# Optimization experiments

Measured on AMD Instinct MI355X. Metric: run time of the kernel, lower is better.

## Reference

```python
import jax, jax.numpy as jnp
import numpy as np

B, T, C = 4, 2048, 1024
H, D = 16, 64  # n_head, head_dim; H*D == C
EPS = 1e-12


def _l2norm(x):
    # matches torch F.normalize(dim=-1): x / max(||x||_2, eps)
    n = jnp.sqrt(jnp.sum(x * x, axis=-1, keepdims=True))
    return x / jnp.maximum(n, EPS)


def setup_inputs() -> dict:
    key = jax.random.key(0)
    ks = jax.random.split(key, 8)
    s = 0.02
    return {
        "x": jax.random.normal(ks[0], (B, T, C), dtype=jnp.float32),
        "Wq": jax.random.normal(ks[1], (C, C), dtype=jnp.float32) * s,
        "Wk": jax.random.normal(ks[2], (C, C), dtype=jnp.float32) * s,
        "Wv": jax.random.normal(ks[3], (C, C), dtype=jnp.float32) * s,
        "Wbeta": jax.random.normal(ks[4], (H, C), dtype=jnp.float32) * s,
        "bbeta": jnp.zeros((H,), dtype=jnp.float32),
        "Wgate": jax.random.normal(ks[5], (C, C), dtype=jnp.float32) * s,
        "Wo": jax.random.normal(ks[6], (C, C), dtype=jnp.float32) * s,
    }


def _forward(x, Wq, Wk, Wv, Wbeta, bbeta, Wgate, Wo):
    q = (x @ Wq.T).reshape(B, T, H, D)
    k = (x @ Wk.T).reshape(B, T, H, D)
    v = (x @ Wv.T).reshape(B, T, H, D)
    beta = jax.nn.sigmoid(x @ Wbeta.T + bbeta)  # (B,T,H)
    gate = jax.nn.sigmoid(x @ Wgate.T)          # (B,T,C)

    q = _l2norm(q)
    k = _l2norm(k)

    # time-major for scan: (T,B,H,D) / (T,B,H)
    qT = jnp.transpose(q, (1, 0, 2, 3))
    kT = jnp.transpose(k, (1, 0, 2, 3))
    vT = jnp.transpose(v, (1, 0, 2, 3))
    bT = jnp.transpose(beta, (1, 0, 2))

    M0 = jnp.zeros((B, H, D, D), dtype=x.dtype)

    def step(M, inp):
        q_t, k_t, v_t, b_t = inp
        o_t = jnp.einsum('bhdc,bhc->bhd', M, q_t)       # read state with q (pre-update)
        Mk = jnp.einsum('bhdc,bhc->bhd', M, k_t)
        dv = v_t - Mk                                    # delta-rule error
        M = M + b_t[..., None, None] * jnp.einsum('bhd,bhc->bhdc', dv, k_t)
        return M, o_t

    _, oT = jax.lax.scan(step, M0, (qT, kT, vT, bT))     # oT: (T,B,H,D)
    o = jnp.transpose(oT, (1, 0, 2, 3)).reshape(B, T, C)
    return (gate * o) @ Wo.T


def reference(x, Wq, Wk, Wv, Wbeta, bbeta, Wgate, Wo):
    return _forward(x, Wq, Wk, Wv, Wbeta, bbeta, Wgate, Wo)
```

## Files before the change

### kernel.cpp

```cpp
#include <hip/hip_runtime.h>
#include <cstdint>
#include <cstddef>

#define Bz 4
#define Tz 2048
#define Cz 1024
#define Hz 16
#define Dz 64
#define NTOK (Bz*Tz)
#define CHL 32
#define NCH (Tz/CHL)

typedef __attribute__((ext_vector_type(8))) short  short8;
typedef __attribute__((ext_vector_type(4))) float  floatx4;

__device__ __forceinline__ unsigned short f2bf(float x) {
  union { float f; uint32_t u; } a; a.f = x;
  uint32_t r = a.u + 0x7fffu + ((a.u >> 16) & 1u);
  return (unsigned short)(r >> 16);
}
__device__ __forceinline__ float bf2f(unsigned short u) {
  union { uint32_t i; float f; } a; a.i = ((uint32_t)u) << 16; return a.f;
}
__device__ __forceinline__ float sigmoidf_(float z) {
  return 1.0f / (1.0f + __expf(-z));
}
__device__ __forceinline__ uint32_t cvtpk_bf16(float a, float b) {
  uint32_t d;
  asm volatile("v_cvt_pk_bf16_f32 %0, %1, %2" : "=v"(d) : "v"(a), "v"(b));
  return d;
}
__device__ __forceinline__ float lo16f(uint32_t u) {
  union { uint32_t i; float f; } a; a.i = u << 16; return a.f;
}
__device__ __forceinline__ float hi16f(uint32_t u) {
  union { uint32_t i; float f; } a; a.i = u & 0xffff0000u; return a.f;
}

__device__ __forceinline__ void gload_lds16(const void* gptr, void* lptr) {
  __builtin_amdgcn_global_load_lds(
      (const __attribute__((address_space(1))) void*)(uintptr_t)gptr,
      (__attribute__((address_space(3))) void*)(uint32_t)(uintptr_t)lptr,
      16, 0, 0);
}

template<int CTRL>
__device__ __forceinline__ float dpp_addf(float x) {
  int y = __builtin_amdgcn_update_dpp(0, __float_as_int(x), CTRL, 0xF, 0xF, true);
  return x + __int_as_float(y);
}
__device__ __forceinline__ float rowsum16(float x) {
  x = dpp_addf<0xB1>(x);
  x = dpp_addf<0x4E>(x);
  x = dpp_addf<0x124>(x);
  x = dpp_addf<0x128>(x);
  return x;
}

union FragU { uint32_t u[4]; short8 s; };

__global__ __launch_bounds__(256) void cvt_bf16_kernel(const float* __restrict__ in,
                                                       unsigned short* __restrict__ out,
                                                       int n4) {
  int i = blockIdx.x * blockDim.x + threadIdx.x;
  int stride = gridDim.x * blockDim.x;
  const float4* in4 = (const float4*)in;
  ushort4* out4 = (ushort4*)out;
  for (; i < n4; i += stride) {
    float4 f = in4[i];
    ushort4 u;
    u.x = f2bf(f.x); u.y = f2bf(f.y); u.z = f2bf(f.z); u.w = f2bf(f.w);
    out4[i] = u;
  }
}

__global__ __launch_bounds__(256) void cvt_w5_kernel(
    const float* __restrict__ s0, const float* __restrict__ s1,
    const float* __restrict__ s2, const float* __restrict__ s3,
    const float* __restrict__ s4,
    unsigned short* __restrict__ d0, unsigned short* __restrict__ d1,
    unsigned short* __restrict__ d2, unsigned short* __restrict__ d3,
    unsigned short* __restrict__ d4, int n4)
{
  const int w = blockIdx.y;
  const float* s = (w == 0) ? s0 : (w == 1) ? s1 : (w == 2) ? s2 : (w == 3) ? s3 : s4;
  unsigned short* d = (w == 0) ? d0 : (w == 1) ? d1 : (w == 2) ? d2 : (w == 3) ? d3 : d4;
  int i = blockIdx.x * blockDim.x + threadIdx.x;
  if (i < n4) {
    float4 f = ((const float4*)s)[i];
    ushort4 u;
    u.x = f2bf(f.x); u.y = f2bf(f.y); u.z = f2bf(f.z); u.w = f2bf(f.w);
    ((ushort4*)d)[i] = u;
  }
}

#define VM8()  asm volatile("s_waitcnt vmcnt(8)" ::: "memory")
#define VM4()  asm volatile("s_waitcnt vmcnt(4)" ::: "memory")
#define VM0()  asm volatile("s_waitcnt vmcnt(0)" ::: "memory")
#define LGKM0() asm volatile("s_waitcnt lgkmcnt(0)" ::: "memory")
#define BARR() __builtin_amdgcn_s_barrier()

__global__ __launch_bounds__(512, 2) void gemm256_kernel(
    const unsigned short* __restrict__ A,
    const unsigned short* __restrict__ W0, const unsigned short* __restrict__ W1,
    const unsigned short* __restrict__ W2, const unsigned short* __restrict__ W3,
    void* __restrict__ O0, void* __restrict__ O1,
    void* __restrict__ O2, void* __restrict__ O3,
    int M, int N, int K, int nz_sigmoid, int norm_mask, int out_bf16)
{
  __shared__ unsigned short smem[8 * 8192];

  const int gx = gridDim.x, gz = gridDim.z;
  const int nwg = gx * gridDim.y * gz;
  int flat = (blockIdx.z * gridDim.y + blockIdx.y) * gx + blockIdx.x;
  if ((nwg & 7) == 0) flat = (flat & 7) * (nwg >> 3) + (flat >> 3);
  const int xz = gx * gz;
  const int by = flat / xz;
  const int rem = flat - by * xz;
  const int bz = rem / gx;
  const int bx = rem - bz * gx;

  const unsigned short* Bw = (bz == 0) ? W0 : (bz == 1) ? W1 : (bz == 2) ? W2 : W3;
  void* Cw = (bz == 0) ? O0 : (bz == 1) ? O1 : (bz == 2) ? O2 : O3;
  const bool act = (bz == nz_sigmoid);
  const bool donorm = (norm_mask >> bz) & 1;

  const int m0 = by * 256, n0 = bx * 256;
  const int tid = threadIdx.x;
  const int wid = tid >> 6, lane = tid & 63;
  const int wm = wid >> 2, wn = wid & 3;
  const int ml = lane & 15, kq = lane >> 4;

  const unsigned short* Ap = A  + (size_t)m0 * K;
  const unsigned short* Bp = Bw + (size_t)n0 * K;

  const int srow = wid * 16 + (lane >> 2);
  const int ss8  = ((lane & 3) ^ ((lane >> 3) & 3)) * 8;
  const int rs8  = (kq ^ ((ml >> 1) & 3)) * 8;
  const int arow = wm * 128 + ml;
  const int brow = wn * 64 + ml;

  const int NT = K >> 6;
  const int hmax = NT << 2;

  floatx4 acc[8][4];
#pragma unroll
  for (int i = 0; i < 8; ++i)
#pragma unroll
    for (int j = 0; j < 4; ++j) acc[i][j] = floatx4{0.f, 0.f, 0.f, 0.f};

#define STAGE1(hsi) do {                                                      \
    const int ht_ = (hsi) >> 2, hh_ = (hsi) & 3;                              \
    const unsigned short* p_ = (hh_ & 1) ? Bp : Ap;                           \
    const int kb_ = ht_ * 64 + (hh_ >> 1) * 32;                               \
    unsigned short* lb_ = &smem[(((ht_ & 1) << 2) + hh_) * 8192 + wid * 512]; \
    gload_lds16(p_ + (size_t)srow * K + kb_ + ss8, lb_);                      \
    gload_lds16(p_ + (size_t)(128 + srow) * K + kb_ + ss8, lb_ + 4096);       \
  } while (0)

  int hs = 0;
  for (; hs < 6 && hs < hmax; ++hs) STAGE1(hs);
  VM8();
  BARR();

#define LOAD_A(Hb, mh)                                                        \
  _Pragma("unroll") for (int i = 0; i < 4; ++i)                               \
    af[i] = *(const short8*)&Hb[(arow + (mh) * 64 + i * 16) * 32 + rs8];
#define LOAD_B(Hb)                                                            \
  _Pragma("unroll") for (int j = 0; j < 4; ++j)                               \
    bf[j] = *(const short8*)&Hb[(brow + j * 16) * 32 + rs8];
#define MFMA_Q(mh)                                                            \
  __builtin_amdgcn_s_setprio(1);                                              \
  _Pragma("unroll") for (int i = 0; i < 4; ++i)                               \
    _Pragma("unroll") for (int j = 0; j < 4; ++j)                             \
      acc[(mh) * 4 + i][j] = __builtin_amdgcn_mfma_f32_16x16x32_bf16(         \
          af[i], bf[j], acc[(mh) * 4 + i][j], 0, 0, 0);                       \
  __builtin_amdgcn_s_setprio(0);
#define STAGE_NEXT() do { if (hs < hmax) { STAGE1(hs); ++hs; } } while (0)

  short8 af[4], bf[4];
  for (int t = 0; t < NT; ++t) {
    const unsigned short* Ah0 = &smem[(((t & 1) << 2) + 0) * 8192];
    const unsigned short* Bh0 = &smem[(((t & 1) << 2) + 1) * 8192];
    const unsigned short* Ah1 = &smem[(((t & 1) << 2) + 2) * 8192];
    const unsigned short* Bh1 = &smem[(((t & 1) << 2) + 3) * 8192];

    LOAD_A(Ah0, 0); LOAD_B(Bh0);
    STAGE_NEXT();
    BARR(); LGKM0();
    MFMA_Q(0);
    BARR();

    LOAD_A(Ah0, 1);
    STAGE_NEXT();
    BARR(); LGKM0();
    MFMA_Q(1);
    if (t == NT - 1) { VM0(); } else { VM8(); }
    BARR();

    LOAD_A(Ah1, 0); LOAD_B(Bh1);
    STAGE_NEXT();
    BARR(); LGKM0();
    MFMA_Q(0);
    BARR();

    LOAD_A(Ah1, 1);
    STAGE_NEXT();
    BARR(); LGKM0();
    MFMA_Q(1);
    if (t < NT - 2) { VM8(); } else if (t == NT - 2) { VM4(); }
    BARR();
  }

  float scale[8][4];
  if (donorm) {
#pragma unroll
    for (int i = 0; i < 8; ++i) {
#pragma unroll
      for (int r = 0; r < 4; ++r) {
        float ss = 0.f;
#pragma unroll
        for (int j = 0; j < 4; ++j) ss = fmaf(acc[i][j][r], acc[i][j][r], ss);
        ss = rowsum16(ss);
        scale[i][r] = 1.0f / fmaxf(sqrtf(ss), 1e-12f);
      }
    }
  }

  const int row_base = m0 + wm * 128;
  const int col_base = n0 + wn * 64;
#pragma unroll
  for (int i = 0; i < 8; ++i) {
#pragma unroll
    for (int j = 0; j < 4; ++j) {
      const int col = col_base + j * 16 + ml;
#pragma unroll
      for (int r = 0; r < 4; ++r) {
        const int row = row_base + i * 16 + kq * 4 + r;
        float val = acc[i][j][r];
        if (donorm) val *= scale[i][r];
        if (act) val = sigmoidf_(val);
        if (out_bf16) ((unsigned short*)Cw)[(size_t)row * N + col] = f2bf(val);
        else          ((float*)Cw)[(size_t)row * N + col] = val;
      }
    }
  }
}

__global__ __launch_bounds__(256) void beta_kernel(
    const float* __restrict__ x, const float* __restrict__ Wb,
    const float* __restrict__ bb, float* __restrict__ beta_out)
{
  const int n = blockIdx.x;
  const int wid = threadIdx.x >> 6;
  const int lane = threadIdx.x & 63;
  const float* xr = x + (size_t)n * Cz;
  for (int h = wid; h < Hz; h += 4) {
    const float* wr = Wb + (size_t)h * Cz;
    float s = 0.f;
#pragma unroll 4
    for (int i = lane; i < Cz; i += 64) s = fmaf(xr[i], wr[i], s);
#pragma unroll
    for (int ofs = 32; ofs >= 1; ofs >>= 1) s += __shfl_xor(s, ofs);
    if (lane == 0) beta_out[(size_t)n * Hz + h] = sigmoidf_(s + bb[h]);
  }
}


__global__ __launch_bounds__(256) void deltachunk_phase1(
    const unsigned short* __restrict__ qb, const unsigned short* __restrict__ kb,
    const unsigned short* __restrict__ vb, const float* __restrict__ betaf,
    float* __restrict__ of,
    unsigned short* __restrict__ qtb, unsigned short* __restrict__ wbuf,
    unsigned short* __restrict__ ubuf, unsigned short* __restrict__ ktb)
{
  __shared__ unsigned short Kb[32][72], Qb[32][72], Vb[32][72];
  __shared__ float As[32][33];
  __shared__ unsigned short Sb[32][40];
  __shared__ unsigned short Us[32][72], Ws[32][72], Qts[32][72];
  __shared__ float bsh[32];

  const int bid = blockIdx.x;
  const int chain = bid & 63;
  const int chunk = bid >> 6;
  const int b = chain >> 4, h = chain & 15;
  const int tid = threadIdx.x;
  const int wid = tid >> 6, lane = tid & 63;
  const int ml = lane & 15, kq = lane >> 4;

  const size_t tok0 = (size_t)b * Tz + (size_t)chunk * CHL;
  const size_t cb = ((size_t)chain * NCH + chunk) * 2048;

  {
    const int row = tid >> 3, c8 = (tid & 7) * 8;
    const size_t ga = (tok0 + row) * Cz + h * Dz + c8;
    *(uint4*)&Qb[row][c8] = *(const uint4*)&qb[ga];
    *(uint4*)&Kb[row][c8] = *(const uint4*)&kb[ga];
    *(uint4*)&Vb[row][c8] = *(const uint4*)&vb[ga];
  }
  if (tid < 32) bsh[tid] = betaf[(tok0 + tid) * Hz + h];
  __syncthreads();

  {
    const int tr = wid & 1, tc = wid >> 1;
    floatx4 accA = {0.f,0.f,0.f,0.f}, accS = {0.f,0.f,0.f,0.f};
#pragma unroll
    for (int eh = 0; eh < 2; ++eh) {
      short8 ka = *(const short8*)&Kb[tr * 16 + ml][eh * 32 + kq * 8];
      short8 kbf = *(const short8*)&Kb[tc * 16 + ml][eh * 32 + kq * 8];
      short8 qa = *(const short8*)&Qb[tr * 16 + ml][eh * 32 + kq * 8];
      accA = __builtin_amdgcn_mfma_f32_16x16x32_bf16(ka, kbf, accA, 0, 0, 0);
      accS = __builtin_amdgcn_mfma_f32_16x16x32_bf16(qa, kbf, accS, 0, 0, 0);
    }
#pragma unroll
    for (int r = 0; r < 4; ++r) {
      int t = tr * 16 + kq * 4 + r;
      int s = tc * 16 + ml;
      As[t][s] = bsh[t] * accA[r];
      Sb[t][s] = (t > s) ? f2bf(accS[r]) : (unsigned short)0;
    }
  }
  __syncthreads();

  if (tid < 128) {
    const int j = tid;
    float x[32];
    if (j < 64) {
#pragma unroll
      for (int t = 0; t < 32; ++t) x[t] = bsh[t] * bf2f(Vb[t][j]);
    } else {
#pragma unroll
      for (int t = 0; t < 32; ++t) x[t] = bsh[t] * bf2f(Kb[t][j - 64]);
    }
#pragma unroll
    for (int t = 0; t < 31; ++t) {
      float xt = x[t];
#pragma unroll
      for (int s = t + 1; s < 32; ++s) x[s] = fmaf(-As[s][t], xt, x[s]);
    }
    if (j < 64) {
#pragma unroll
      for (int t = 0; t < 32; ++t) Us[t][j] = f2bf(x[t]);
    } else {
#pragma unroll
      for (int t = 0; t < 32; ++t) Ws[t][j - 64] = f2bf(x[t]);
    }
  }
  __syncthreads();

  {
    const int dw = wid * 16 + ml;
    FragU bu, bw;
#pragma unroll
    for (int r = 0; r < 4; ++r) {
      bu.u[r] = (uint32_t)Us[kq * 8 + 2 * r][dw] | ((uint32_t)Us[kq * 8 + 2 * r + 1][dw] << 16);
      bw.u[r] = (uint32_t)Ws[kq * 8 + 2 * r][dw] | ((uint32_t)Ws[kq * 8 + 2 * r + 1][dw] << 16);
    }
    floatx4 accO[2], accQ[2];
#pragma unroll
    for (int tt = 0; tt < 2; ++tt) { accO[tt] = floatx4{0.f,0.f,0.f,0.f}; accQ[tt] = floatx4{0.f,0.f,0.f,0.f}; }
#pragma unroll
    for (int tt = 0; tt < 2; ++tt) {
      short8 sa = *(const short8*)&Sb[tt * 16 + ml][kq * 8];
      accO[tt] = __builtin_amdgcn_mfma_f32_16x16x32_bf16(sa, bu.s, accO[tt], 0, 0, 0);
      accQ[tt] = __builtin_amdgcn_mfma_f32_16x16x32_bf16(sa, bw.s, accQ[tt], 0, 0, 0);
    }
#pragma unroll
    for (int tt = 0; tt < 2; ++tt) {
#pragma unroll
      for (int r = 0; r < 4; ++r) {
        int t = tt * 16 + kq * 4 + r;
        of[(tok0 + t) * Cz + h * Dz + dw] = accO[tt][r];
        Qts[t][dw] = f2bf(bf2f(Qb[t][dw]) - accQ[tt][r]);
      }
    }
  }

  unsigned short ktmp[8], utmp[8];
  {
    const int e = tid >> 2, tq = (tid & 3) * 8;
#pragma unroll
    for (int i2 = 0; i2 < 8; ++i2) { ktmp[i2] = Kb[tq + i2][e]; utmp[i2] = Us[tq + i2][e]; }
  }
  __syncthreads();

  {
    const int row = tid >> 3, c8 = (tid & 7) * 8;
    const size_t o16 = cb + (size_t)row * 64 + c8;
    *(uint4*)&qtb[o16]  = *(const uint4*)&Qts[row][c8];
    *(uint4*)&wbuf[o16] = *(const uint4*)&Ws[row][c8];
    const int e = tid >> 2, tq = (tid & 3) * 8;
    *(uint4*)&ktb[cb + (size_t)e * 32 + tq]  = *(const uint4*)ktmp;
    *(uint4*)&ubuf[cb + (size_t)e * 32 + tq] = *(const uint4*)utmp;
  }
}

__global__ __launch_bounds__(256) void deltachunk_phase2(
    const unsigned short* __restrict__ qtb, const unsigned short* __restrict__ wbuf,
    const unsigned short* __restrict__ ubuf, const unsigned short* __restrict__ ktb,
    float* __restrict__ o2)
{
  __shared__ unsigned short Gb[2][64][72];
  __shared__ unsigned short Ub[2][32][40];
  __shared__ unsigned short Kts[2][64][40];
  __shared__ unsigned short Mh[2][32][72], Ml[2][32][72];

  const int chain = blockIdx.x >> 1;
  const int dh = blockIdx.x & 1;
  const int b = chain >> 4, h = chain & 15;
  const int d0 = dh * 32;
  const int tid = threadIdx.x;
  const int wid = tid >> 6, lane = tid & 63;
  const int ml = lane & 15, kq = lane >> 4;
  const int iq = wid >> 1, jq = wid & 1;

  const size_t cbase = (size_t)chain * NCH * 2048;

  const int grow = tid >> 2;
  const int gc16 = (tid & 3) * 16;
  const int ke   = tid >> 2;
  const int kc8  = (tid & 3) * 8;
  const int ue   = tid >> 3;
  const int uc4  = (tid & 7) * 4;

  const unsigned short* gsrc = (grow < 32) ? qtb : wbuf;
  const size_t gsoff = (size_t)(grow & 31) * 64 + gc16;

  {
    *(uint4*)&Gb[0][grow][gc16]     = *(const uint4*)&gsrc[cbase + gsoff];
    *(uint4*)&Gb[0][grow][gc16 + 8] = *(const uint4*)&gsrc[cbase + gsoff + 8];
    *(uint4*)&Kts[0][ke][kc8]       = *(const uint4*)&ktb[cbase + (size_t)ke * 32 + kc8];
    *(uint2*)&Ub[0][ue][uc4]        = *(const uint2*)&ubuf[cbase + (size_t)(d0 + ue) * 32 + uc4];
  }
  for (int i = tid; i < 32 * 72; i += 256) { (&Mh[0][0][0])[i] = 0; (&Ml[0][0][0])[i] = 0; }
  __syncthreads();

  const int idxA = (ml + 16 * ((kq & 1) * 2)) * 4;
  const int idxB = (ml + 16 * ((kq & 1) * 2 + 1)) * 4;
  const bool hiKq = (kq >= 2);

  floatx4 mAcc[4];
#pragma unroll
  for (int a = 0; a < 4; ++a) mAcc[a] = floatx4{0.f, 0.f, 0.f, 0.f};

  for (int c = 0; c < NCH; ++c) {
    const int cbuf = c & 1, nbuf = cbuf ^ 1;
    const int mr = c & 1, mw = mr ^ 1;
    const size_t tok0 = (size_t)b * Tz + (size_t)c * CHL;

    const int cn = (c + 1 < NCH) ? c + 1 : c;
    const size_t cbn = cbase + (size_t)cn * 2048;
    uint4 sg0 = *(const uint4*)&gsrc[cbn + gsoff];
    uint4 sg1 = *(const uint4*)&gsrc[cbn + gsoff + 8];
    uint4 sk  = *(const uint4*)&ktb[cbn + (size_t)ke * 32 + kc8];
    uint2 su  = *(const uint2*)&ubuf[cbn + (size_t)(d0 + ue) * 32 + uc4];

    floatx4 g1[2];
    g1[0] = floatx4{0.f,0.f,0.f,0.f}; g1[1] = floatx4{0.f,0.f,0.f,0.f};
#pragma unroll
    for (int eh = 0; eh < 2; ++eh) {
      short8 afr0 = *(const short8*)&Gb[cbuf][iq * 32 + 0  + ml][eh * 32 + kq * 8];
      short8 afr1 = *(const short8*)&Gb[cbuf][iq * 32 + 16 + ml][eh * 32 + kq * 8];
      short8 bh = *(const short8*)&Mh[mr][jq * 16 + ml][eh * 32 + kq * 8];
      short8 bl = *(const short8*)&Ml[mr][jq * 16 + ml][eh * 32 + kq * 8];
      g1[0] = __builtin_amdgcn_mfma_f32_16x16x32_bf16(afr0, bh, g1[0], 0, 0, 0);
      g1[0] = __builtin_amdgcn_mfma_f32_16x16x32_bf16(afr0, bl, g1[0], 0, 0, 0);
      g1[1] = __builtin_amdgcn_mfma_f32_16x16x32_bf16(afr1, bh, g1[1], 0, 0, 0);
      g1[1] = __builtin_amdgcn_mfma_f32_16x16x32_bf16(afr1, bl, g1[1], 0, 0, 0);
    }

    if (iq == 0) {
#pragma unroll
      for (int ti = 0; ti < 2; ++ti)
#pragma unroll
        for (int r = 0; r < 4; ++r)
          o2[(tok0 + ti * 16 + kq * 4 + r) * Cz + h * Dz + d0 + jq * 16 + ml] = g1[ti][r];
    } else {
      uint32_t pkh[2][2], pkl[2][2];
#pragma unroll
      for (int ti = 0; ti < 2; ++ti) {
        ushort4 uu = *(const ushort4*)&Ub[cbuf][jq * 16 + ml][ti * 16 + kq * 4];
        float z0 = bf2f(uu.x) - g1[ti][0];
        float z1 = bf2f(uu.y) - g1[ti][1];
        float z2 = bf2f(uu.z) - g1[ti][2];
        float z3 = bf2f(uu.w) - g1[ti][3];
        uint32_t h01 = cvtpk_bf16(z0, z1), h23 = cvtpk_bf16(z2, z3);
        pkh[ti][0] = h01; pkh[ti][1] = h23;
        pkl[ti][0] = cvtpk_bf16(z0 - lo16f(h01), z1 - hi16f(h01));
        pkl[ti][1] = cvtpk_bf16(z2 - lo16f(h23), z3 - hi16f(h23));
      }
      FragU zh, zl;
#pragma unroll
      for (int s = 0; s < 4; ++s) {
        const int idx = (s < 2) ? idxA : idxB;
        const int rp = s & 1;
        int v0 = __builtin_amdgcn_ds_bpermute(idx, (int)pkh[0][rp]);
        int v1 = __builtin_amdgcn_ds_bpermute(idx, (int)pkh[1][rp]);
        zh.u[s] = hiKq ? (uint32_t)v1 : (uint32_t)v0;
        int w0 = __builtin_amdgcn_ds_bpermute(idx, (int)pkl[0][rp]);
        int w1 = __builtin_amdgcn_ds_bpermute(idx, (int)pkl[1][rp]);
        zl.u[s] = hiKq ? (uint32_t)w1 : (uint32_t)w0;
      }
#pragma unroll
      for (int et = 0; et < 4; ++et) {
        short8 kfr = *(const short8*)&Kts[cbuf][et * 16 + ml][kq * 8];
        mAcc[et] = __builtin_amdgcn_mfma_f32_16x16x32_bf16(kfr, zh.s, mAcc[et], 0, 0, 0);
        mAcc[et] = __builtin_amdgcn_mfma_f32_16x16x32_bf16(kfr, zl.s, mAcc[et], 0, 0, 0);
      }
#pragma unroll
      for (int et = 0; et < 4; ++et) {
        float m0 = mAcc[et][0], m1 = mAcc[et][1], m2 = mAcc[et][2], m3 = mAcc[et][3];
        uint32_t h01 = cvtpk_bf16(m0, m1), h23 = cvtpk_bf16(m2, m3);
        uint32_t l01 = cvtpk_bf16(m0 - lo16f(h01), m1 - hi16f(h01));
        uint32_t l23 = cvtpk_bf16(m2 - lo16f(h23), m3 - hi16f(h23));
        *(uint2*)&Mh[mw][jq * 16 + ml][et * 16 + kq * 4] = make_uint2(h01, h23);
        *(uint2*)&Ml[mw][jq * 16 + ml][et * 16 + kq * 4] = make_uint2(l01, l23);
      }
    }

    *(uint4*)&Gb[nbuf][grow][gc16]     = sg0;
    *(uint4*)&Gb[nbuf][grow][gc16 + 8] = sg1;
    *(uint4*)&Kts[nbuf][ke][kc8]       = sk;
    *(uint2*)&Ub[nbuf][ue][uc4]        = su;

    LGKM0();
    BARR();
  }
}

__global__ __launch_bounds__(256) void gate_mul_kernel(
    const unsigned short* __restrict__ gsig, const float* __restrict__ o,
    const float* __restrict__ o2v, unsigned short* __restrict__ out, int n4)
{
  int i = blockIdx.x * blockDim.x + threadIdx.x;
  int stride = gridDim.x * blockDim.x;
  const ushort4* g4 = (const ushort4*)gsig;
  const float4* o4 = (const float4*)o;
  const float4* p4 = (const float4*)o2v;
  ushort4* out4 = (ushort4*)out;
  for (; i < n4; i += stride) {
    ushort4 gv = g4[i];
    float4 ov = o4[i];
    float4 pv = p4[i];
    ushort4 u;
    u.x = f2bf(bf2f(gv.x) * (ov.x + pv.x));
    u.y = f2bf(bf2f(gv.y) * (ov.y + pv.y));
    u.z = f2bf(bf2f(gv.z) * (ov.z + pv.z));
    u.w = f2bf(bf2f(gv.w) * (ov.w + pv.w));
    out4[i] = u;
  }
}

extern "C" void kernel_launch(void* const* d_in, const int* in_sizes, int n_in,
                              void* d_out, int out_size, void* d_ws, size_t ws_size,
                              hipStream_t stream) {
  const float* x     = (const float*)d_in[0];
  const float* Wq    = (const float*)d_in[1];
  const float* Wk    = (const float*)d_in[2];
  const float* Wv    = (const float*)d_in[3];
  const float* Wbeta = (const float*)d_in[4];
  const float* bbeta = (const float*)d_in[5];
  const float* Wgate = (const float*)d_in[6];
  const float* Wo    = (const float*)d_in[7];
  float* out = (float*)d_out;

  char* ws = (char*)d_ws;
  size_t off = 0;
  auto alloc = [&](size_t bytes) -> char* {
    char* p = ws + off;
    off += (bytes + 255) & ~(size_t)255;
    return p;
  };
  unsigned short* xb  = (unsigned short*)alloc((size_t)NTOK * Cz * 2);
  unsigned short* Wqb = (unsigned short*)alloc((size_t)Cz * Cz * 2);
  unsigned short* Wkb = (unsigned short*)alloc((size_t)Cz * Cz * 2);
  unsigned short* Wvb = (unsigned short*)alloc((size_t)Cz * Cz * 2);
  unsigned short* Wgb = (unsigned short*)alloc((size_t)Cz * Cz * 2);
  unsigned short* Wob = (unsigned short*)alloc((size_t)Cz * Cz * 2);
  unsigned short* qb  = (unsigned short*)alloc((size_t)NTOK * Cz * 2);
  unsigned short* kb  = (unsigned short*)alloc((size_t)NTOK * Cz * 2);
  unsigned short* vb  = (unsigned short*)alloc((size_t)NTOK * Cz * 2);
  unsigned short* gb  = (unsigned short*)alloc((size_t)NTOK * Cz * 2);
  float* of    = (float*)alloc((size_t)NTOK * Cz * 4);
  float* o2    = (float*)alloc((size_t)NTOK * Cz * 4);
  float* betaf = (float*)alloc((size_t)NTOK * Hz * 4);
  unsigned short* qtb  = (unsigned short*)alloc((size_t)64 * NCH * 2048 * 2);
  unsigned short* wbuf = (unsigned short*)alloc((size_t)64 * NCH * 2048 * 2);
  unsigned short* ubuf = (unsigned short*)alloc((size_t)64 * NCH * 2048 * 2);
  unsigned short* ktb  = (unsigned short*)alloc((size_t)64 * NCH * 2048 * 2);
  unsigned short* ab = xb;

  const int n4x = NTOK * Cz / 4;
  const int n4w = Cz * Cz / 4;

  cvt_bf16_kernel<<<dim3(1024), dim3(256), 0, stream>>>(x, xb, n4x);
  cvt_w5_kernel<<<dim3(n4w / 256, 5), dim3(256), 0, stream>>>(
      Wq, Wk, Wv, Wgate, Wo, Wqb, Wkb, Wvb, Wgb, Wob, n4w);

  gemm256_kernel<<<dim3(Cz / 256, NTOK / 256, 4), dim3(512), 0, stream>>>(
      xb, Wqb, Wkb, Wvb, Wgb, qb, kb, vb, gb, NTOK, Cz, Cz, 3, 3, 1);

  beta_kernel<<<dim3(NTOK), dim3(256), 0, stream>>>(x, Wbeta, bbeta, betaf);

  deltachunk_phase1<<<dim3(64 * NCH), dim3(256), 0, stream>>>(
      qb, kb, vb, betaf, of, qtb, wbuf, ubuf, ktb);
  deltachunk_phase2<<<dim3(128), dim3(256), 0, stream>>>(qtb, wbuf, ubuf, ktb, o2);

  gate_mul_kernel<<<dim3(1024), dim3(256), 0, stream>>>(gb, of, o2, ab, n4x);

  gemm256_kernel<<<dim3(Cz / 256, NTOK / 256, 1), dim3(512), 0, stream>>>(
      ab, Wob, Wob, Wob, Wob, out, out, out, out, NTOK, Cz, Cz, -1, 0, 0);
}
```

Baseline: 374.0 us.

## Template GEMM tile width, stage epilogue through LDS, transpose triangular-solve matrix

Templates the GEMM on N-tile width and output type. The output projection now uses a 128-wide tile, which doubles its workgroup count for better CU occupancy on the final fp32 GEMM. The epilogue now stages results through shared memory so each thread writes full 16-byte rows instead of scattered scalar stores. In the chunked delta kernel, the As matrix is stored transposed with padding so the forward-substitution loop reads contiguous rows. The extra LDS round-trips and barriers in the epilogue add cost.

```diff
diff --git a/kernel.cpp b/kernel.cpp
--- a/kernel.cpp
+++ b/kernel.cpp
@@ -95,20 +95,28 @@
 }
 
 #define VM8()  asm volatile("s_waitcnt vmcnt(8)" ::: "memory")
+#define VM6()  asm volatile("s_waitcnt vmcnt(6)" ::: "memory")
 #define VM4()  asm volatile("s_waitcnt vmcnt(4)" ::: "memory")
+#define VM3()  asm volatile("s_waitcnt vmcnt(3)" ::: "memory")
 #define VM0()  asm volatile("s_waitcnt vmcnt(0)" ::: "memory")
 #define LGKM0() asm volatile("s_waitcnt lgkmcnt(0)" ::: "memory")
 #define BARR() __builtin_amdgcn_s_barrier()
 
+template<int BN, int OB16>
 __global__ __launch_bounds__(512, 2) void gemm256_kernel(
     const unsigned short* __restrict__ A,
     const unsigned short* __restrict__ W0, const unsigned short* __restrict__ W1,
     const unsigned short* __restrict__ W2, const unsigned short* __restrict__ W3,
     void* __restrict__ O0, void* __restrict__ O1,
     void* __restrict__ O2, void* __restrict__ O3,
-    int M, int N, int K, int nz_sigmoid, int norm_mask, int out_bf16)
+    int M, int N, int K, int nz_sigmoid, int norm_mask)
 {
-  __shared__ unsigned short smem[8 * 8192];
+  constexpr int LB  = (BN == 256) ? 2 : 1;
+  constexpr int NJ  = BN / 64;
+  constexpr int AH  = 8192;
+  constexpr int BH  = BN * 32;
+  constexpr int PAR = 2 * AH + 2 * BH;
+  __shared__ unsigned short smem[2 * PAR];
 
   const int gx = gridDim.x, gz = gridDim.z;
   const int nwg = gx * gridDim.y * gz;
@@ -125,7 +133,7 @@
   const bool act = (bz == nz_sigmoid);
   const bool donorm = (norm_mask >> bz) & 1;
 
-  const int m0 = by * 256, n0 = bx * 256;
+  const int m0 = by * 256, n0 = bx * BN;
   const int tid = threadIdx.x;
   const int wid = tid >> 6, lane = tid & 63;
   const int wm = wid >> 2, wn = wid & 3;
@@ -138,52 +146,55 @@
   const int ss8  = ((lane & 3) ^ ((lane >> 3) & 3)) * 8;
   const int rs8  = (kq ^ ((ml >> 1) & 3)) * 8;
   const int arow = wm * 128 + ml;
-  const int brow = wn * 64 + ml;
+  const int brow = wn * (BN / 4) + ml;
 
   const int NT = K >> 6;
   const int hmax = NT << 2;
 
-  floatx4 acc[8][4];
+  floatx4 acc[8][NJ];
 #pragma unroll
   for (int i = 0; i < 8; ++i)
 #pragma unroll
-    for (int j = 0; j < 4; ++j) acc[i][j] = floatx4{0.f, 0.f, 0.f, 0.f};
-
+    for (int j = 0; j < NJ; ++j) acc[i][j] = floatx4{0.f, 0.f, 0.f, 0.f};
+
+#define HOFF(hh) ((hh) == 0 ? 0 : (hh) == 1 ? AH : (hh) == 2 ? AH + BH : 2 * AH + BH)
 #define STAGE1(hsi) do {                                                      \
     const int ht_ = (hsi) >> 2, hh_ = (hsi) & 3;                              \
-    const unsigned short* p_ = (hh_ & 1) ? Bp : Ap;                           \
+    const bool isB_ = hh_ & 1;                                                \
+    const unsigned short* p_ = isB_ ? Bp : Ap;                                \
     const int kb_ = ht_ * 64 + (hh_ >> 1) * 32;                               \
-    unsigned short* lb_ = &smem[(((ht_ & 1) << 2) + hh_) * 8192 + wid * 512]; \
+    unsigned short* lb_ = &smem[(ht_ & 1) * PAR + HOFF(hh_) + wid * 512];     \
     gload_lds16(p_ + (size_t)srow * K + kb_ + ss8, lb_);                      \
-    gload_lds16(p_ + (size_t)(128 + srow) * K + kb_ + ss8, lb_ + 4096);       \
+    if (!isB_ || LB == 2)                                                     \
+      gload_lds16(p_ + (size_t)(128 + srow) * K + kb_ + ss8, lb_ + 4096);     \
   } while (0)
 
   int hs = 0;
   for (; hs < 6 && hs < hmax; ++hs) STAGE1(hs);
-  VM8();
+  if constexpr (BN == 256) { VM8(); } else { VM6(); }
   BARR();
 
 #define LOAD_A(Hb, mh)                                                        \
   _Pragma("unroll") for (int i = 0; i < 4; ++i)                               \
     af[i] = *(const short8*)&Hb[(arow + (mh) * 64 + i * 16) * 32 + rs8];
 #define LOAD_B(Hb)                                                            \
-  _Pragma("unroll") for (int j = 0; j < 4; ++j)                               \
+  _Pragma("unroll") for (int j = 0; j < NJ; ++j)                              \
     bf[j] = *(const short8*)&Hb[(brow + j * 16) * 32 + rs8];
 #define MFMA_Q(mh)                                                            \
   __builtin_amdgcn_s_setprio(1);                                              \
   _Pragma("unroll") for (int i = 0; i < 4; ++i)                               \
-    _Pragma("unroll") for (int j = 0; j < 4; ++j)                             \
+    _Pragma("unroll") for (int j = 0; j < NJ; ++j)                            \
       acc[(mh) * 4 + i][j] = __builtin_amdgcn_mfma_f32_16x16x32_bf16(         \
           af[i], bf[j], acc[(mh) * 4 + i][j], 0, 0, 0);                       \
   __builtin_amdgcn_s_setprio(0);
 #define STAGE_NEXT() do { if (hs < hmax) { STAGE1(hs); ++hs; } } while (0)
 
-  short8 af[4], bf[4];
+  short8 af[4], bf[NJ];
   for (int t = 0; t < NT; ++t) {
-    const unsigned short* Ah0 = &smem[(((t & 1) << 2) + 0) * 8192];
-    const unsigned short* Bh0 = &smem[(((t & 1) << 2) + 1) * 8192];
-    const unsigned short* Ah1 = &smem[(((t & 1) << 2) + 2) * 8192];
-    const unsigned short* Bh1 = &smem[(((t & 1) << 2) + 3) * 8192];
+    const unsigned short* Ah0 = &smem[(t & 1) * PAR + HOFF(0)];
+    const unsigned short* Bh0 = &smem[(t & 1) * PAR + HOFF(1)];
+    const unsigned short* Ah1 = &smem[(t & 1) * PAR + HOFF(2)];
+    const unsigned short* Bh1 = &smem[(t & 1) * PAR + HOFF(3)];
 
     LOAD_A(Ah0, 0); LOAD_B(Bh0);
     STAGE_NEXT();
@@ -195,7 +206,8 @@
     STAGE_NEXT();
     BARR(); LGKM0();
     MFMA_Q(1);
-    if (t == NT - 1) { VM0(); } else { VM8(); }
+    if (t == NT - 1) { VM0(); }
+    else { if constexpr (BN == 256) { VM8(); } else { VM6(); } }
     BARR();
 
     LOAD_A(Ah1, 0); LOAD_B(Bh1);
@@ -208,7 +220,8 @@
     STAGE_NEXT();
     BARR(); LGKM0();
     MFMA_Q(1);
-    if (t < NT - 2) { VM8(); } else if (t == NT - 2) { VM4(); }
+    if (t < NT - 2) { if constexpr (BN == 256) { VM8(); } else { VM6(); } }
+    else if (t == NT - 2) { if constexpr (BN == 256) { VM4(); } else { VM3(); } }
     BARR();
   }
 
@@ -220,29 +233,56 @@
       for (int r = 0; r < 4; ++r) {
         float ss = 0.f;
 #pragma unroll
-        for (int j = 0; j < 4; ++j) ss = fmaf(acc[i][j][r], acc[i][j][r], ss);
+        for (int j = 0; j < NJ; ++j) ss = fmaf(acc[i][j][r], acc[i][j][r], ss);
         ss = rowsum16(ss);
         scale[i][r] = 1.0f / fmaxf(sqrtf(ss), 1e-12f);
       }
     }
   }
 
-  const int row_base = m0 + wm * 128;
-  const int col_base = n0 + wn * 64;
-#pragma unroll
-  for (int i = 0; i < 8; ++i) {
-#pragma unroll
-    for (int j = 0; j < 4; ++j) {
-      const int col = col_base + j * 16 + ml;
-#pragma unroll
-      for (int r = 0; r < 4; ++r) {
-        const int row = row_base + i * 16 + kq * 4 + r;
-        float val = acc[i][j][r];
-        if (donorm) val *= scale[i][r];
-        if (act) val = sigmoidf_(val);
-        if (out_bf16) ((unsigned short*)Cw)[(size_t)row * N + col] = f2bf(val);
-        else          ((float*)Cw)[(size_t)row * N + col] = val;
-      }
+  {
+    unsigned short* eps = smem;
+    float* epf = (float*)smem;
+    const int row_r = tid >> 2;
+    const int seg = tid & 3;
+#pragma unroll
+    for (int rh = 0; rh < 2; ++rh) {
+      if (wm == rh) {
+#pragma unroll
+        for (int i = 0; i < 8; ++i) {
+#pragma unroll
+          for (int j = 0; j < NJ; ++j) {
+#pragma unroll
+            for (int r = 0; r < 4; ++r) {
+              float val = acc[i][j][r];
+              if (donorm) val *= scale[i][r];
+              if (act) val = sigmoidf_(val);
+              const int er = i * 16 + kq * 4 + r;
+              const int ec = wn * (BN / 4) + j * 16 + ml;
+              if constexpr (OB16) eps[er * 264 + ec] = f2bf(val);
+              else                epf[er * 132 + ec] = val;
+            }
+          }
+        }
+      }
+      LGKM0(); BARR();
+      const int grow_ = m0 + rh * 128 + row_r;
+      if constexpr (OB16) {
+#pragma unroll
+        for (int kk = 0; kk < BN / 32; ++kk) {
+          const int c = kk * 32 + seg * 8;
+          uint4 v = *(const uint4*)&eps[row_r * 264 + c];
+          *(uint4*)&((unsigned short*)Cw)[(size_t)grow_ * N + n0 + c] = v;
+        }
+      } else {
+#pragma unroll
+        for (int kk = 0; kk < BN / 16; ++kk) {
+          const int c = kk * 16 + seg * 4;
+          uint4 v = *(const uint4*)&epf[row_r * 132 + c];
+          *(uint4*)&((float*)Cw)[(size_t)grow_ * N + n0 + c] = v;
+        }
+      }
+      LGKM0(); BARR();
     }
   }
 }
@@ -266,7 +306,6 @@
   }
 }
 
-
 __global__ __launch_bounds__(256) void deltachunk_phase1(
     const unsigned short* __restrict__ qb, const unsigned short* __restrict__ kb,
     const unsigned short* __restrict__ vb, const float* __restrict__ betaf,
@@ -275,7 +314,7 @@
     unsigned short* __restrict__ ubuf, unsigned short* __restrict__ ktb)
 {
   __shared__ unsigned short Kb[32][72], Qb[32][72], Vb[32][72];
-  __shared__ float As[32][33];
+  __shared__ float As[32][36];
   __shared__ unsigned short Sb[32][40];
   __shared__ unsigned short Us[32][72], Ws[32][72], Qts[32][72];
   __shared__ float bsh[32];
@@ -316,7 +355,7 @@
     for (int r = 0; r < 4; ++r) {
       int t = tr * 16 + kq * 4 + r;
       int s = tc * 16 + ml;
-      As[t][s] = bsh[t] * accA[r];
+      As[s][t] = bsh[t] * accA[r];
       Sb[t][s] = (t > s) ? f2bf(accS[r]) : (unsigned short)0;
     }
   }
@@ -336,7 +375,7 @@
     for (int t = 0; t < 31; ++t) {
       float xt = x[t];
 #pragma unroll
-      for (int s = t + 1; s < 32; ++s) x[s] = fmaf(-As[s][t], xt, x[s]);
+      for (int s = t + 1; s < 32; ++s) x[s] = fmaf(-As[t][s], xt, x[s]);
     }
     if (j < 64) {
 #pragma unroll
@@ -597,8 +636,8 @@
   cvt_w5_kernel<<<dim3(n4w / 256, 5), dim3(256), 0, stream>>>(
       Wq, Wk, Wv, Wgate, Wo, Wqb, Wkb, Wvb, Wgb, Wob, n4w);
 
-  gemm256_kernel<<<dim3(Cz / 256, NTOK / 256, 4), dim3(512), 0, stream>>>(
-      xb, Wqb, Wkb, Wvb, Wgb, qb, kb, vb, gb, NTOK, Cz, Cz, 3, 3, 1);
+  gemm256_kernel<256, 1><<<dim3(Cz / 256, NTOK / 256, 4), dim3(512), 0, stream>>>(
+      xb, Wqb, Wkb, Wvb, Wgb, qb, kb, vb, gb, NTOK, Cz, Cz, 3, 3);
 
   beta_kernel<<<dim3(NTOK), dim3(256), 0, stream>>>(x, Wbeta, bbeta, betaf);
 
@@ -608,6 +647,6 @@
 
   gate_mul_kernel<<<dim3(1024), dim3(256), 0, stream>>>(gb, of, o2, ab, n4x);
 
-  gemm256_kernel<<<dim3(Cz / 256, NTOK / 256, 1), dim3(512), 0, stream>>>(
-      ab, Wob, Wob, Wob, Wob, out, out, out, out, NTOK, Cz, Cz, -1, 0, 0);
-}
+  gemm256_kernel<128, 0><<<dim3(Cz / 128, NTOK / 256, 1), dim3(512), 0, stream>>>(
+      ab, Wob, Wob, Wob, Wob, out, out, out, out, NTOK, Cz, Cz, -1, 0);
+}
```

Result: slower. 387.9 us (+3.7%).
